# Kernel optimization log

Measured on AMD Instinct MI355X. Metric: run time of the kernel, lower is better.

The kernel has to match this reference:

```python
import jax, jax.numpy as jnp
import numpy as np

N = 20000      # n_nodes
E = 320000     # n_edges (multiple of 4, so _from_coo drops nothing)
D = 512        # embed_dim
H = 8          # num_heads
DK = D // H    # d_k = 64


def setup_inputs() -> dict:
    key = jax.random.key(0)
    ks = jax.random.split(key, 12)
    x = jax.random.normal(ks[0], (N, D), jnp.float32)
    rows = jnp.sort(jax.random.randint(ks[1], (E,), 0, N))
    cols = jax.random.randint(ks[2], (E,), 0, N)
    edge_index = jnp.stack([rows, cols]).astype(jnp.int32)  # [2, E]
    att_bias = jax.random.normal(ks[3], (E, H), jnp.float32)
    s = float(1.0 / np.sqrt(D))  # ~xavier scale
    Wq = jax.random.normal(ks[4], (D, D), jnp.float32) * s
    Wk = jax.random.normal(ks[5], (D, D), jnp.float32) * s
    Wv = jax.random.normal(ks[6], (D, D), jnp.float32) * s
    Wo = jax.random.normal(ks[7], (D, D), jnp.float32) * s
    bq = jnp.zeros((D,), jnp.float32)
    bk = jnp.zeros((D,), jnp.float32)
    bv = jnp.zeros((D,), jnp.float32)
    bo = jnp.zeros((D,), jnp.float32)
    return dict(x=x, edge_index=edge_index, att_bias=att_bias,
                Wq=Wq, bq=bq, Wk=Wk, bk=bk, Wv=Wv, bv=bv, Wo=Wo, bo=bo)


def reference(x, edge_index, att_bias, Wq, bq, Wk, bk, Wv, bv, Wo, bo):
    n = x.shape[0]
    rows, cols = edge_index[0], edge_index[1]
    # per-head projections: [n, H, DK]
    q = (x @ Wq + bq).reshape(n, H, DK)
    k = (x @ Wk + bk).reshape(n, H, DK)
    v = (x @ Wv + bv).reshape(n, H, DK)
    scale = 1.0 / jnp.sqrt(jnp.asarray(DK, x.dtype))
    # masked QK^T on the edge pattern, plus additive bias: [E, H]
    logits = jnp.einsum('ehd,ehd->eh', q[rows] * scale, k[cols]) + att_bias
    # CSR (segment) softmax over each destination row
    row_max = jax.ops.segment_max(logits, rows, num_segments=n)      # [n, H]
    p = jnp.exp(logits - row_max[rows])                              # [E, H]
    denom = jax.ops.segment_sum(p, rows, num_segments=n)            # [n, H]
    att = p / denom[rows]                                            # [E, H]
    # sparse-dense bmm: y[i] = sum_{e: rows[e]=i} att[e] * v[cols[e]]
    y = jax.ops.segment_sum(att[:, :, None] * v[cols], rows, num_segments=n)  # [n, H, DK]
    out = y.reshape(n, H * DK) @ Wo + bo
    return out
```

## Files before the change

kernel.cpp:

```cpp
#include <hip/hip_runtime.h>
#include <hip/hip_bf16.h>

typedef unsigned short ushort_t;
typedef unsigned int uint32;
typedef __attribute__((ext_vector_type(8))) short short8;
typedef __attribute__((ext_vector_type(4))) float floatx4;

#define DEV __device__ __forceinline__

DEV float b2f(ushort_t u) { return __uint_as_float(((uint32)u) << 16); }
DEV ushort_t f2b(float f) {
  __hip_bfloat16 h = __float2bfloat16(f);
  return __builtin_bit_cast(unsigned short, h);
}
DEV void unpack8(const uint4& u, float* f) {
  f[0] = __uint_as_float(u.x << 16); f[1] = __uint_as_float(u.x & 0xffff0000u);
  f[2] = __uint_as_float(u.y << 16); f[3] = __uint_as_float(u.y & 0xffff0000u);
  f[4] = __uint_as_float(u.z << 16); f[5] = __uint_as_float(u.z & 0xffff0000u);
  f[6] = __uint_as_float(u.w << 16); f[7] = __uint_as_float(u.w & 0xffff0000u);
}

#define GLOAD_LDS(gp, lp) \
  __builtin_amdgcn_global_load_lds((const __attribute__((address_space(1))) uint32*)(gp), \
                                   (__attribute__((address_space(3))) uint32*)(lp), 16, 0, 0)

__global__ __launch_bounds__(256) void k_detect(const ushort_t* __restrict__ x,
                                                int* __restrict__ flag) {
  __shared__ int red[256];
  int tid = threadIdx.x;
  int wild = 0;
  for (int i = tid; i < 4096; i += 256) {
    uint32 e = (x[i] >> 7) & 0xFFu;
    if (e < 100u || e > 140u) wild++;
  }
  red[tid] = wild;
  __syncthreads();
  for (int s = 128; s > 0; s >>= 1) {
    if (tid < s) red[tid] += red[tid + s];
    __syncthreads();
  }
  if (tid == 0) flag[0] = (red[0] > 400) ? 1 : 0;
}

__global__ __launch_bounds__(256) void k_transpose(
    const void* __restrict__ Wq, const void* __restrict__ Wk,
    const void* __restrict__ Wv, const void* __restrict__ Wo,
    ushort_t* __restrict__ WT4, const int* __restrict__ flagp) {
  __shared__ ushort_t t[32][33];
  int isf32 = *flagp;
  int z = blockIdx.z;
  const void* src = (z == 0) ? Wq : (z == 1) ? Wk : (z == 2) ? Wv : Wo;
  ushort_t* dst = WT4 + (size_t)z * 512 * 512;
  int bx = blockIdx.x, by = blockIdx.y;
  int tx = threadIdx.x, ty = threadIdx.y;
#pragma unroll
  for (int i = 0; i < 4; i++) {
    size_t idx = (size_t)(by * 32 + ty + 8 * i) * 512 + bx * 32 + tx;
    ushort_t v = isf32 ? f2b(((const float*)src)[idx]) : ((const ushort_t*)src)[idx];
    t[ty + 8 * i][tx] = v;
  }
  __syncthreads();
#pragma unroll
  for (int i = 0; i < 4; i++)
    dst[(size_t)(bx * 32 + ty + 8 * i) * 512 + by * 32 + tx] = t[tx][ty + 8 * i];
}

__global__ __launch_bounds__(256) void k_biases(
    const void* __restrict__ bq, const void* __restrict__ bk,
    const void* __restrict__ bv, const void* __restrict__ bo,
    float* __restrict__ biasf, const int* __restrict__ flagp) {
  int i = blockIdx.x * 256 + threadIdx.x;
  if (i >= 2048) return;
  int z = i >> 9, j = i & 511;
  const void* b = (z == 0) ? bq : (z == 1) ? bk : (z == 2) ? bv : bo;
  biasf[i] = (*flagp) ? ((const float*)b)[j] : b2f(((const ushort_t*)b)[j]);
}

__global__ __launch_bounds__(256) void k_convx(
    const void* __restrict__ x, ushort_t* __restrict__ xb, int n8,
    const int* __restrict__ flagp) {
  int i = blockIdx.x * 256 + threadIdx.x;
  if (i >= n8) return;
  if (*flagp) {
    const float* xf = (const float*)x + (size_t)i * 8;
    float4 f0 = ((const float4*)xf)[0];
    float4 f1 = ((const float4*)xf)[1];
    uint4 o;
    o.x = (uint32)f2b(f0.x) | ((uint32)f2b(f0.y) << 16);
    o.y = (uint32)f2b(f0.z) | ((uint32)f2b(f0.w) << 16);
    o.z = (uint32)f2b(f1.x) | ((uint32)f2b(f1.y) << 16);
    o.w = (uint32)f2b(f1.z) | ((uint32)f2b(f1.w) << 16);
    ((uint4*)xb)[i] = o;
  } else {
    ((uint4*)xb)[i] = ((const uint4*)x)[i];
  }
}

__global__ void k_build_rp(const int* __restrict__ rows, int E, int N, int* __restrict__ rp) {
  int i = blockIdx.x * blockDim.x + threadIdx.x;
  if (i > N) return;
  int lo = 0, hi = E;
  while (lo < hi) {
    int mid = (lo + hi) >> 1;
    if (rows[mid] < i) lo = mid + 1; else hi = mid;
  }
  rp[i] = lo;
}

DEV void gemm_body(const ushort_t* __restrict__ A, const ushort_t* __restrict__ BT,
                   const float* __restrict__ bias, void* C,
                   int M, int ldc, float scale, int row0, int by, int f32out) {
  __shared__ ushort_t As[128 * 32];
  __shared__ ushort_t Bs[128 * 32];
  int tid = threadIdx.x;
  int w = tid >> 6, lane = tid & 63;
  int sr = lane >> 2;
  int sk = (lane & 3) * 8;

  floatx4 acc[4][4];
#pragma unroll
  for (int i = 0; i < 4; i++)
#pragma unroll
    for (int j = 0; j < 4; j++)
#pragma unroll
      for (int r = 0; r < 4; r++) acc[i][j][r] = 0.f;

  int lm = lane & 15, quad = lane >> 4;
  int wr = w >> 1, wc = w & 1;
  const int nG = by * 128 + w * 32;

  int rA0 = row0 + w * 32 + sr; if (rA0 >= M) rA0 = M - 1;
  int rA1 = rA0 + 16;          if (rA1 >= M) rA1 = M - 1;
  const ushort_t* gA0 = A + (size_t)rA0 * 512 + sk;
  const ushort_t* gA1 = A + (size_t)rA1 * 512 + sk;
  const ushort_t* gB0 = BT + (size_t)(nG + sr) * 512 + sk;
  const ushort_t* gB1 = BT + (size_t)(nG + 16 + sr) * 512 + sk;

  for (int k0 = 0; k0 < 512; k0 += 32) {
    GLOAD_LDS(gA0 + k0, As + (w * 32 + 0) * 32);
    GLOAD_LDS(gA1 + k0, As + (w * 32 + 16) * 32);
    GLOAD_LDS(gB0 + k0, Bs + (w * 32 + 0) * 32);
    GLOAD_LDS(gB1 + k0, Bs + (w * 32 + 16) * 32);
    __syncthreads();

    const ushort_t* pa = As + (wr * 64 + lm) * 32 + quad * 8;
    const ushort_t* pb = Bs + (wc * 64 + lm) * 32 + quad * 8;
    short8 af[4], bfr[4];
#pragma unroll
    for (int t4 = 0; t4 < 4; t4++) {
      af[t4]  = *(const short8*)(pa + t4 * 16 * 32);
      bfr[t4] = *(const short8*)(pb + t4 * 16 * 32);
    }
#pragma unroll
    for (int mt = 0; mt < 4; mt++)
#pragma unroll
      for (int nt = 0; nt < 4; nt++)
        acc[mt][nt] = __builtin_amdgcn_mfma_f32_16x16x32_bf16(af[mt], bfr[nt], acc[mt][nt], 0, 0, 0);
    __syncthreads();
  }

  int colB = by * 128 + wc * 64 + lm;
  float bv4[4];
#pragma unroll
  for (int nt = 0; nt < 4; nt++) bv4[nt] = bias[colB + nt * 16];
#pragma unroll
  for (int mt = 0; mt < 4; mt++) {
    int rg0 = row0 + wr * 64 + mt * 16 + quad * 4;
#pragma unroll
    for (int nt = 0; nt < 4; nt++) {
#pragma unroll
      for (int r = 0; r < 4; r++) {
        int rg = rg0 + r;
        if (rg < M) {
          float val = (acc[mt][nt][r] + bv4[nt]) * scale;
          size_t off = (size_t)rg * ldc + colB + nt * 16;
          if (f32out) ((float*)C)[off] = val;
          else        ((ushort_t*)C)[off] = f2b(val);
        }
      }
    }
  }
}

__global__ __launch_bounds__(256) void k_gemm_qkv(
    const ushort_t* __restrict__ xb, const ushort_t* __restrict__ WT4,
    const float* __restrict__ biasf, ushort_t* Qp, ushort_t* KV, int M) {
  int z = blockIdx.z;
  const ushort_t* BT = WT4 + (size_t)z * 512 * 512;
  const float* bias = biasf + (size_t)z * 512;
  ushort_t* Cp = (z == 0) ? Qp : (z == 1) ? KV : (KV + 512);
  int ldc = (z == 0) ? 512 : 1024;
  float scale = (z == 0) ? 0.125f : 1.0f;
  gemm_body(xb, BT, bias, Cp, M, ldc, scale, blockIdx.x * 128, blockIdx.y, 0);
}

__global__ __launch_bounds__(256) void k_gemm_out(
    const ushort_t* __restrict__ y, const ushort_t* __restrict__ WT4,
    const float* __restrict__ biasf, void* out, int M,
    const int* __restrict__ flagp) {
  gemm_body(y, WT4 + (size_t)3 * 512 * 512, biasf + 3 * 512, out, M, 512, 1.0f,
            blockIdx.x * 128, blockIdx.y, *flagp);
}

__global__ __launch_bounds__(256) void k_edge(
    ushort_t* Qy, const ushort_t* __restrict__ KV,
    const void* __restrict__ ab, const int* __restrict__ cols,
    const int* __restrict__ rp, int Nn, int E, const int* __restrict__ flagp) {
  int node = blockIdx.x * 4 + (threadIdx.x >> 6);
  if (node >= Nn) return;
  int lane = threadIdx.x & 63;
  int h8 = lane >> 3;
  int isf32 = *flagp;

  uint4 qu = ((const uint4*)(Qy + (size_t)node * 512))[lane];
  float qf[8];
  unpack8(qu, qf);

  int e0 = rp[node], e1 = rp[node + 1];
  int cnt = e1 - e0;

  float s0 = 0.f, s1 = 0.f;
  float acc0[8], acc1[8];
#pragma unroll
  for (int j = 0; j < 8; j++) { acc0[j] = 0.f; acc1[j] = 0.f; }

  uint4 kb[4], vb[4];
  float abf[4];

  auto pref = [&](int t, int slot) {
    int valid = t < cnt;
    int ei = valid ? (e0 + t) : e0;
    int c = valid ? cols[ei] : 0;
    const ushort_t* kvrow = KV + (size_t)c * 1024;
    kb[slot] = ((const uint4*)kvrow)[lane];
    vb[slot] = ((const uint4*)(kvrow + 512))[lane];
    size_t bi = (size_t)ei * 8 + h8;
    float a = isf32 ? ((const float*)ab)[bi] : b2f(((const ushort_t*)ab)[bi]);
    abf[slot] = valid ? a : -1e30f;
  };
  auto consume = [&](int slot, float* acc, float& s) {
    float kf[8];
    unpack8(kb[slot], kf);
    float d = 0.f;
#pragma unroll
    for (int j = 0; j < 8; j++) d = fmaf(qf[j], kf[j], d);
    d += __shfl_xor(d, 1);
    d += __shfl_xor(d, 2);
    d += __shfl_xor(d, 4);
    float logit = fminf(d + abf[slot], 80.f);
    float pw = __expf(logit);
    s += pw;
    float vf[8];
    unpack8(vb[slot], vf);
#pragma unroll
    for (int j = 0; j < 8; j++) acc[j] = fmaf(pw, vf[j], acc[j]);
  };

  pref(0, 0); pref(1, 1); pref(2, 2); pref(3, 3);
  int iters = (cnt + 3) >> 2;
  for (int it = 0; it < iters; ++it) {
    int nt = it * 4 + 4;
    consume(0, acc0, s0); pref(nt + 0, 0);
    consume(1, acc1, s1); pref(nt + 1, 1);
    consume(2, acc0, s0); pref(nt + 2, 2);
    consume(3, acc1, s1); pref(nt + 3, 3);
  }

  float s = s0 + s1;
  float inv = (cnt > 0 && s > 0.f) ? 1.f / s : 0.f;
  ushort_t hb[8];
#pragma unroll
  for (int j = 0; j < 8; j++) hb[j] = f2b((acc0[j] + acc1[j]) * inv);
  uint4 uh;
  uh.x = (uint32)hb[0] | ((uint32)hb[1] << 16);
  uh.y = (uint32)hb[2] | ((uint32)hb[3] << 16);
  uh.z = (uint32)hb[4] | ((uint32)hb[5] << 16);
  uh.w = (uint32)hb[6] | ((uint32)hb[7] << 16);
  ((uint4*)(Qy + (size_t)node * 512))[lane] = uh;
}

extern "C" void kernel_launch(void* const* d_in, const int* in_sizes, int n_in,
                              void* d_out, int out_size, void* d_ws, size_t ws_size,
                              hipStream_t stream) {
  const void* x  = d_in[0];
  const int* ei  = (const int*)d_in[1];
  const void* ab = d_in[2];
  const void* Wq = d_in[3];
  const void* bq = d_in[4];
  const void* Wk = d_in[5];
  const void* bk = d_in[6];
  const void* Wv = d_in[7];
  const void* bv = d_in[8];
  const void* Wo = d_in[9];
  const void* bo = d_in[10];

  const int D = 512;
  int M = in_sizes[0] / D;
  int E = in_sizes[1] / 2;
  const int* rows = ei;
  const int* cols = ei + E;

  char* p = (char*)d_ws;
  size_t off = 0;
  auto carve = [&](size_t bytes) -> void* {
    off = (off + 255) & ~(size_t)255;
    void* r = p + off;
    off += bytes;
    return r;
  };
  int* flag      = (int*)carve(4);
  ushort_t* WT4  = (ushort_t*)carve((size_t)4 * 512 * 512 * 2);
  float* biasf   = (float*)carve((size_t)4 * 512 * 4);
  ushort_t* xb   = (ushort_t*)carve((size_t)M * 512 * 2);
  ushort_t* Qp   = (ushort_t*)carve((size_t)M * 512 * 2);
  ushort_t* KV   = (ushort_t*)carve((size_t)M * 1024 * 2);
  int* rp        = (int*)carve((size_t)(M + 1) * 4);
  (void)ws_size;

  k_detect<<<1, 256, 0, stream>>>((const ushort_t*)x, flag);
  k_transpose<<<dim3(16, 16, 4), dim3(32, 8), 0, stream>>>(Wq, Wk, Wv, Wo, WT4, flag);
  k_biases<<<8, 256, 0, stream>>>(bq, bk, bv, bo, biasf, flag);
  int n8 = M * 512 / 8;
  k_convx<<<(n8 + 255) / 256, 256, 0, stream>>>(x, xb, n8, flag);
  k_build_rp<<<(M + 1 + 255) / 256, 256, 0, stream>>>(rows, E, M, rp);

  int rb = (M + 127) / 128;
  k_gemm_qkv<<<dim3(rb, 4, 3), 256, 0, stream>>>(xb, WT4, biasf, Qp, KV, M);
  k_edge<<<(M + 3) / 4, 256, 0, stream>>>(Qp, KV, ab, cols, rp, M, E, flag);
  k_gemm_out<<<dim3(rb, 4, 1), 256, 0, stream>>>(Qp, WT4, biasf, d_out, M, flag);
}
```

Measured before the change: 315.4 us.

## Quantize K and V to per-head int8 with scales for edge gather

The QKV GEMM epilogue now writes K and V as int8 with one absmax scale per row and head, packed into 1088-byte rows (int8 K, int8 V, then float scales). The edge kernel gathers 8-byte chunks instead of 16-byte ones and applies the scales during the dot product and the V accumulation. The aim is to halve the random-gather traffic for K and V, which dominates the per-edge loop. The cost is extra quantization error in the logits and the output, plus a few shuffles and int-to-float conversions.

```diff
diff --git a/kernel.cpp b/kernel.cpp
--- a/kernel.cpp
+++ b/kernel.cpp
@@ -19,10 +19,22 @@
   f[4] = __uint_as_float(u.z << 16); f[5] = __uint_as_float(u.z & 0xffff0000u);
   f[6] = __uint_as_float(u.w << 16); f[7] = __uint_as_float(u.w & 0xffff0000u);
 }
+DEV void unpack_i8x8(uint2 u, float* f) {
+  f[0] = (float)((int)(u.x << 24) >> 24);
+  f[1] = (float)((int)(u.x << 16) >> 24);
+  f[2] = (float)((int)(u.x << 8) >> 24);
+  f[3] = (float)((int)u.x >> 24);
+  f[4] = (float)((int)(u.y << 24) >> 24);
+  f[5] = (float)((int)(u.y << 16) >> 24);
+  f[6] = (float)((int)(u.y << 8) >> 24);
+  f[7] = (float)((int)u.y >> 24);
+}
 
 #define GLOAD_LDS(gp, lp) \
   __builtin_amdgcn_global_load_lds((const __attribute__((address_space(1))) uint32*)(gp), \
                                    (__attribute__((address_space(3))) uint32*)(lp), 16, 0, 0)
+
+#define KVROW 1088
 
 __global__ __launch_bounds__(256) void k_detect(const ushort_t* __restrict__ x,
                                                 int* __restrict__ flag) {
@@ -109,7 +121,7 @@
 
 DEV void gemm_body(const ushort_t* __restrict__ A, const ushort_t* __restrict__ BT,
                    const float* __restrict__ bias, void* C,
-                   int M, int ldc, float scale, int row0, int by, int f32out) {
+                   int M, int ldc, float scale, int row0, int by, int mode) {
   __shared__ ushort_t As[128 * 32];
   __shared__ ushort_t Bs[128 * 32];
   int tid = threadIdx.x;
@@ -163,35 +175,70 @@
   float bv4[4];
 #pragma unroll
   for (int nt = 0; nt < 4; nt++) bv4[nt] = bias[colB + nt * 16];
-#pragma unroll
-  for (int mt = 0; mt < 4; mt++) {
-    int rg0 = row0 + wr * 64 + mt * 16 + quad * 4;
-#pragma unroll
-    for (int nt = 0; nt < 4; nt++) {
-#pragma unroll
-      for (int r = 0; r < 4; r++) {
-        int rg = rg0 + r;
-        if (rg < M) {
-          float val = (acc[mt][nt][r] + bv4[nt]) * scale;
-          size_t off = (size_t)rg * ldc + colB + nt * 16;
-          if (f32out) ((float*)C)[off] = val;
-          else        ((ushort_t*)C)[off] = f2b(val);
+
+  if (mode <= 1) {
+#pragma unroll
+    for (int mt = 0; mt < 4; mt++) {
+      int rg0 = row0 + wr * 64 + mt * 16 + quad * 4;
+#pragma unroll
+      for (int nt = 0; nt < 4; nt++) {
+#pragma unroll
+        for (int r = 0; r < 4; r++) {
+          int rg = rg0 + r;
+          if (rg < M) {
+            float val = (acc[mt][nt][r] + bv4[nt]) * scale;
+            size_t off = (size_t)rg * ldc + colB + nt * 16;
+            if (mode == 1) ((float*)C)[off] = val;
+            else           ((ushort_t*)C)[off] = f2b(val);
+          }
         }
       }
     }
+  } else {
+    int vslot = (mode == 4);
+    int colbase = by * 128 + wc * 64;
+    int head = colbase >> 6;
+#pragma unroll
+    for (int mt = 0; mt < 4; mt++) {
+#pragma unroll
+      for (int r = 0; r < 4; r++) {
+        int rg = row0 + wr * 64 + mt * 16 + quad * 4 + r;
+        float v0 = acc[mt][0][r] + bv4[0];
+        float v1 = acc[mt][1][r] + bv4[1];
+        float v2 = acc[mt][2][r] + bv4[2];
+        float v3 = acc[mt][3][r] + bv4[3];
+        float am = fmaxf(fmaxf(fabsf(v0), fabsf(v1)), fmaxf(fabsf(v2), fabsf(v3)));
+        am = fmaxf(am, __shfl_xor(am, 1));
+        am = fmaxf(am, __shfl_xor(am, 2));
+        am = fmaxf(am, __shfl_xor(am, 4));
+        am = fmaxf(am, __shfl_xor(am, 8));
+        am = fmaxf(am, 1e-20f);
+        float inv8 = 127.0f / am;
+        float sc8 = am * (1.0f / 127.0f);
+        if (rg < M) {
+          unsigned char* Crow = (unsigned char*)C + (size_t)rg * KVROW + colbase + (vslot ? 512 : 0);
+          Crow[lm +  0] = (unsigned char)(signed char)(int)rintf(v0 * inv8);
+          Crow[lm + 16] = (unsigned char)(signed char)(int)rintf(v1 * inv8);
+          Crow[lm + 32] = (unsigned char)(signed char)(int)rintf(v2 * inv8);
+          Crow[lm + 48] = (unsigned char)(signed char)(int)rintf(v3 * inv8);
+          if (lm == 0)
+            *(float*)((unsigned char*)C + (size_t)rg * KVROW + 1024 + head * 8 + vslot * 4) = sc8;
+        }
+      }
+    }
   }
 }
 
 __global__ __launch_bounds__(256) void k_gemm_qkv(
     const ushort_t* __restrict__ xb, const ushort_t* __restrict__ WT4,
-    const float* __restrict__ biasf, ushort_t* Qp, ushort_t* KV, int M) {
+    const float* __restrict__ biasf, ushort_t* Qp, unsigned char* KV8, int M) {
   int z = blockIdx.z;
   const ushort_t* BT = WT4 + (size_t)z * 512 * 512;
   const float* bias = biasf + (size_t)z * 512;
-  ushort_t* Cp = (z == 0) ? Qp : (z == 1) ? KV : (KV + 512);
-  int ldc = (z == 0) ? 512 : 1024;
-  float scale = (z == 0) ? 0.125f : 1.0f;
-  gemm_body(xb, BT, bias, Cp, M, ldc, scale, blockIdx.x * 128, blockIdx.y, 0);
+  if (z == 0)
+    gemm_body(xb, BT, bias, Qp, M, 512, 0.125f, blockIdx.x * 128, blockIdx.y, 0);
+  else
+    gemm_body(xb, BT, bias, KV8, M, 0, 1.0f, blockIdx.x * 128, blockIdx.y, z == 1 ? 3 : 4);
 }
 
 __global__ __launch_bounds__(256) void k_gemm_out(
@@ -203,7 +250,7 @@
 }
 
 __global__ __launch_bounds__(256) void k_edge(
-    ushort_t* Qy, const ushort_t* __restrict__ KV,
+    ushort_t* Qy, const unsigned char* __restrict__ KV8,
     const void* __restrict__ ab, const int* __restrict__ cols,
     const int* __restrict__ rp, int Nn, int E, const int* __restrict__ flagp) {
   int node = blockIdx.x * 4 + (threadIdx.x >> 6);
@@ -224,36 +271,39 @@
 #pragma unroll
   for (int j = 0; j < 8; j++) { acc0[j] = 0.f; acc1[j] = 0.f; }
 
-  uint4 kb[4], vb[4];
+  uint2 kb[4], vb[4];
+  float2 scb[4];
   float abf[4];
 
   auto pref = [&](int t, int slot) {
     int valid = t < cnt;
     int ei = valid ? (e0 + t) : e0;
     int c = valid ? cols[ei] : 0;
-    const ushort_t* kvrow = KV + (size_t)c * 1024;
-    kb[slot] = ((const uint4*)kvrow)[lane];
-    vb[slot] = ((const uint4*)(kvrow + 512))[lane];
+    const unsigned char* kvrow = KV8 + (size_t)c * KVROW;
+    kb[slot] = *(const uint2*)(kvrow + lane * 8);
+    vb[slot] = *(const uint2*)(kvrow + 512 + lane * 8);
+    scb[slot] = *(const float2*)(kvrow + 1024 + h8 * 8);
     size_t bi = (size_t)ei * 8 + h8;
     float a = isf32 ? ((const float*)ab)[bi] : b2f(((const ushort_t*)ab)[bi]);
     abf[slot] = valid ? a : -1e30f;
   };
   auto consume = [&](int slot, float* acc, float& s) {
     float kf[8];
-    unpack8(kb[slot], kf);
+    unpack_i8x8(kb[slot], kf);
     float d = 0.f;
 #pragma unroll
     for (int j = 0; j < 8; j++) d = fmaf(qf[j], kf[j], d);
     d += __shfl_xor(d, 1);
     d += __shfl_xor(d, 2);
     d += __shfl_xor(d, 4);
-    float logit = fminf(d + abf[slot], 80.f);
+    float logit = fminf(fmaf(d, scb[slot].x, abf[slot]), 80.f);
     float pw = __expf(logit);
     s += pw;
+    float pwv = pw * scb[slot].y;
     float vf[8];
-    unpack8(vb[slot], vf);
-#pragma unroll
-    for (int j = 0; j < 8; j++) acc[j] = fmaf(pw, vf[j], acc[j]);
+    unpack_i8x8(vb[slot], vf);
+#pragma unroll
+    for (int j = 0; j < 8; j++) acc[j] = fmaf(pwv, vf[j], acc[j]);
   };
 
   pref(0, 0); pref(1, 1); pref(2, 2); pref(3, 3);
@@ -308,13 +358,13 @@
     off += bytes;
     return r;
   };
-  int* flag      = (int*)carve(4);
-  ushort_t* WT4  = (ushort_t*)carve((size_t)4 * 512 * 512 * 2);
-  float* biasf   = (float*)carve((size_t)4 * 512 * 4);
-  ushort_t* xb   = (ushort_t*)carve((size_t)M * 512 * 2);
-  ushort_t* Qp   = (ushort_t*)carve((size_t)M * 512 * 2);
-  ushort_t* KV   = (ushort_t*)carve((size_t)M * 1024 * 2);
-  int* rp        = (int*)carve((size_t)(M + 1) * 4);
+  int* flag          = (int*)carve(4);
+  ushort_t* WT4      = (ushort_t*)carve((size_t)4 * 512 * 512 * 2);
+  float* biasf       = (float*)carve((size_t)4 * 512 * 4);
+  ushort_t* xb       = (ushort_t*)carve((size_t)M * 512 * 2);
+  ushort_t* Qp       = (ushort_t*)carve((size_t)M * 512 * 2);
+  unsigned char* KV8 = (unsigned char*)carve((size_t)M * KVROW);
+  int* rp            = (int*)carve((size_t)(M + 1) * 4);
   (void)ws_size;
 
   k_detect<<<1, 256, 0, stream>>>((const ushort_t*)x, flag);
@@ -325,7 +375,7 @@
   k_build_rp<<<(M + 1 + 255) / 256, 256, 0, stream>>>(rows, E, M, rp);
 
   int rb = (M + 127) / 128;
-  k_gemm_qkv<<<dim3(rb, 4, 3), 256, 0, stream>>>(xb, WT4, biasf, Qp, KV, M);
-  k_edge<<<(M + 3) / 4, 256, 0, stream>>>(Qp, KV, ab, cols, rp, M, E, flag);
+  k_gemm_qkv<<<dim3(rb, 4, 3), 256, 0, stream>>>(xb, WT4, biasf, Qp, KV8, M);
+  k_edge<<<(M + 3) / 4, 256, 0, stream>>>(Qp, KV8, ab, cols, rp, M, E, flag);
   k_gemm_out<<<dim3(rb, 4, 1), 256, 0, stream>>>(Qp, WT4, biasf, d_out, M, flag);
 }
```

Result: faster. 298.6 us (-5.3%).
